# Performance work log

Measured on AMD Instinct MI355X. Metric: run time of the kernel, lower is better.

The kernel has to match this reference:

```python
import jax, jax.numpy as jnp
import numpy as np

SR = 48000
HARMONIC_NUM = 8          # -> 9 harmonics total
SINE_AMP = 0.1
NOISE_STD = 0.003
VOICED_THRESHOLD = 0.0
B, T, UPP = 8, 2000, 480
S = T * UPP


def setup_inputs() -> dict:
    key = jax.random.key(0)
    k_f0, k_mask, k_ri, k_noise = jax.random.split(key, 4)
    f0 = jax.random.uniform(k_f0, (B, 1, T), jnp.float32, 80.0, 500.0)
    voiced = (jax.random.uniform(k_mask, (B, 1, T)) > 0.2).astype(jnp.float32)
    f0 = f0 * voiced
    # random initial phases; harmonic 0 gets phase 0 (as in torch code)
    rand_ini = jax.random.uniform(k_ri, (B, HARMONIC_NUM + 1), jnp.float32)
    rand_ini = rand_ini.at[:, 0].set(0.0)
    noise_raw = jax.random.normal(k_noise, (B, S), jnp.float32)
    # linear mixing layer: weight = 1/(H+1), bias = 0 per nn.init in __init__
    w = jnp.full((HARMONIC_NUM + 1,), 1.0 / (HARMONIC_NUM + 1), jnp.float32)
    b = jnp.zeros((1,), jnp.float32)
    return {"f0": f0, "rand_ini": rand_ini, "noise_raw": noise_raw,
            "w": w, "b": b, "upp": UPP}


def reference(f0, rand_ini, noise_raw, w, b, upp):
    # f0: [B,1,T] Hz -> nearest-upsample to [B, S]
    f0u = jnp.repeat(f0[:, 0, :], upp, axis=1)              # [B, S]
    uv = (f0u > VOICED_THRESHOLD).astype(f0.dtype)          # [B, S]
    rad = f0u * (2.0 * np.pi / SR)
    # cumsum is linear: one cumsum, broadcast-multiply by harmonic index
    base_phase = jnp.cumsum(rad, axis=1)                    # [B, S]
    mult = jnp.arange(1, HARMONIC_NUM + 2, dtype=f0.dtype)  # [H+1]
    phase = base_phase[:, :, None] * mult + rand_ini[:, None, :] * (2.0 * np.pi)
    sines = jnp.sin(phase) * uv[:, :, None]                 # [B, S, H+1]
    har = jnp.tanh(sines @ w + b[0]) * SINE_AMP             # [B, S]
    noise = noise_raw * NOISE_STD                            # [B, S]
    return har[:, None, :], noise[:, None, :], uv[:, None, :]
```

## Files before the change

### kernel.cpp

```cpp
#include <hip/hip_runtime.h>
#include <hip/hip_bf16.h>
#include <math.h>

constexpr int   B_   = 8;
constexpr int   T_   = 2000;
constexpr int   UPP_ = 480;
constexpr int   S_   = T_ * UPP_;
constexpr int   NH   = 9;
constexpr int   SPT  = 8;
constexpr int   TPR  = S_ / SPT;
constexpr int   NT   = B_ * TPR;
constexpr float INV_SR = 1.0f / 48000.0f;

__global__ __launch_bounds__(256) void frame_scan_kernel(
    const float* __restrict__ f0,
    float2* __restrict__ ftab)
{
    __shared__ double wsum[4];
    const int b    = blockIdx.x;
    const int j    = threadIdx.x;
    const int lane = j & 63;
    const int wid  = j >> 6;
    constexpr int CH = 8;
    const int t0 = j * CH;

    float fc[CH];
    double local = 0.0;
    #pragma unroll
    for (int k = 0; k < CH; ++k) {
        int t = t0 + k;
        float v = (t < T_) ? f0[b * T_ + t] : 0.0f;
        fc[k] = v * INV_SR;
        local += (double)fc[k] * (double)UPP_;
    }

    double x = local;
    #pragma unroll
    for (int off = 1; off < 64; off <<= 1) {
        double y = __shfl_up(x, off, 64);
        if (lane >= off) x += y;
    }
    if (lane == 63) wsum[wid] = x;
    __syncthreads();

    double woff = 0.0;
    #pragma unroll
    for (int w = 0; w < 3; ++w)
        if (w < wid) woff += wsum[w];

    double excl = (x + woff) - local;

    #pragma unroll
    for (int k = 0; k < CH; ++k) {
        int t = t0 + k;
        if (t < T_) {
            double ph = excl - floor(excl);
            ftab[b * T_ + t] = make_float2((float)ph, fc[k]);
            excl += (double)fc[k] * (double)UPP_;
        }
    }
}

__global__ __launch_bounds__(256) void synth_kernel(
    const float* __restrict__ rand_ini,
    const float* __restrict__ noise_raw,
    const float* __restrict__ w,
    const float* __restrict__ bb,
    const float2* __restrict__ ftab,
    float* __restrict__ out)
{
    int g = blockIdx.x * blockDim.x + threadIdx.x;
    if (g >= NT) return;

    int b  = g / TPR;
    int r  = g - b * TPR;
    int s0 = r * SPT;
    int t  = s0 / UPP_;
    int i0 = s0 - t * UPP_;

    float2 pf   = ftab[b * T_ + t];
    float  Pred = pf.x;
    float  fcyc = pf.y;
    float  uvf  = (fcyc > 0.0f) ? 1.0f : 0.0f;
    float  bias = bb[0];

    const size_t row = (size_t)b * S_ + s0;
    const float4 nz0 = *(const float4*)(noise_raw + row);
    const float4 nz1 = *(const float4*)(noise_raw + row + 4);

    float har[SPT];

    if (uvf > 0.0f) {
        float wr[NH], ri[NH];
        #pragma unroll
        for (int h = 0; h < NH; ++h) {
            wr[h] = w[h];
            ri[h] = rand_ini[b * NH + h];
        }
        #pragma unroll
        for (int k = 0; k < SPT; ++k) {
            float base = Pred + fcyc * (float)(i0 + 1 + k);
            float acc = 0.0f;
            #pragma unroll
            for (int h = 0; h < NH; ++h) {
                float ph = base * (float)(h + 1) + ri[h];
                float fr = ph - floorf(ph);
#if __has_builtin(__builtin_amdgcn_sinf)
                float sv = __builtin_amdgcn_sinf(fr);
#else
                float sv = __sinf(fr * 6.2831853071795864769f);
#endif
                acc = fmaf(sv, wr[h], acc);
            }
            float xx = acc + bias;
            float e  = __expf(2.0f * xx);
            har[k]   = (e - 1.0f) / (e + 1.0f) * 0.1f;
        }
    } else {
        float e  = __expf(2.0f * bias);
        float hv = (e - 1.0f) / (e + 1.0f) * 0.1f;
        #pragma unroll
        for (int k = 0; k < SPT; ++k) har[k] = hv;
    }

    float* harp = out;
    float* nzp  = out + (size_t)B_ * S_;
    float* uvp  = out + (size_t)2 * B_ * S_;

    *(float4*)(harp + row)     = make_float4(har[0], har[1], har[2], har[3]);
    *(float4*)(harp + row + 4) = make_float4(har[4], har[5], har[6], har[7]);
    *(float4*)(nzp + row)      = make_float4(nz0.x * 0.003f, nz0.y * 0.003f,
                                             nz0.z * 0.003f, nz0.w * 0.003f);
    *(float4*)(nzp + row + 4)  = make_float4(nz1.x * 0.003f, nz1.y * 0.003f,
                                             nz1.z * 0.003f, nz1.w * 0.003f);
    *(float4*)(uvp + row)      = make_float4(uvf, uvf, uvf, uvf);
    *(float4*)(uvp + row + 4)  = make_float4(uvf, uvf, uvf, uvf);
}

extern "C" void kernel_launch(void* const* d_in, const int* in_sizes, int n_in,
                              void* d_out, int out_size, void* d_ws, size_t ws_size,
                              hipStream_t stream) {
    const float* f0        = (const float*)d_in[0];
    const float* rand_ini  = (const float*)d_in[1];
    const float* noise_raw = (const float*)d_in[2];
    const float* w         = (const float*)d_in[3];
    const float* bb        = (const float*)d_in[4];

    float2* ftab = (float2*)d_ws;

    frame_scan_kernel<<<B_, 256, 0, stream>>>(f0, ftab);
    synth_kernel<<<(NT + 255) / 256, 256, 0, stream>>>(
        rand_ini, noise_raw, w, bb, ftab, (float*)d_out);
}
```

Measured before the change: 34.45 us.

## Replace per-harmonic sines with Chebyshev recurrence and precomputed phase coefficients

Expands sin(h*theta + phi) as sin(h*theta)cos(phi) + cos(h*theta)sin(phi), so the mixing weights and random phases fold into A/B coefficient tables built once in the scan kernel. The harmonics come from a Chebyshev recurrence seeded by one sin/cos pair per sample, replacing nine transcendental calls and fracts. The change also raises samples per thread to 12 with 320-thread blocks aligned to rows, removes the voiced branch by masking the accumulator with uvf, and uses nontemporal loads and stores. The recurrence can accumulate float error at higher harmonics, and it drops the early skip of work for unvoiced frames.

```diff
diff --git a/kernel.cpp b/kernel.cpp
--- a/kernel.cpp
+++ b/kernel.cpp
@@ -7,14 +7,39 @@
 constexpr int   UPP_ = 480;
 constexpr int   S_   = T_ * UPP_;
 constexpr int   NH   = 9;
-constexpr int   SPT  = 8;
+constexpr int   SPT  = 12;
+constexpr int   BLK  = 320;
 constexpr int   TPR  = S_ / SPT;
-constexpr int   NT   = B_ * TPR;
+constexpr int   BPR  = TPR / BLK;
 constexpr float INV_SR = 1.0f / 48000.0f;
+
+typedef float fx4 __attribute__((ext_vector_type(4)));
+
+#if __has_builtin(__builtin_amdgcn_sinf)
+__device__ __forceinline__ float sinrev(float x) { return __builtin_amdgcn_sinf(x); }
+#else
+__device__ __forceinline__ float sinrev(float x) { return __sinf(x * 6.2831853071795864769f); }
+#endif
+#if __has_builtin(__builtin_amdgcn_cosf)
+__device__ __forceinline__ float cosrev(float x) { return __builtin_amdgcn_cosf(x); }
+#else
+__device__ __forceinline__ float cosrev(float x) { return __cosf(x * 6.2831853071795864769f); }
+#endif
+
+__device__ __forceinline__ void nt_store4(float* p, float a, float b, float c, float d) {
+    fx4 v = {a, b, c, d};
+    __builtin_nontemporal_store(v, (fx4*)p);
+}
+__device__ __forceinline__ fx4 nt_load4(const float* p) {
+    return __builtin_nontemporal_load((const fx4*)p);
+}
 
 __global__ __launch_bounds__(256) void frame_scan_kernel(
     const float* __restrict__ f0,
-    float2* __restrict__ ftab)
+    const float* __restrict__ rand_ini,
+    const float* __restrict__ w,
+    float2* __restrict__ ftab,
+    float2* __restrict__ abtab)
 {
     __shared__ double wsum[4];
     const int b    = blockIdx.x;
@@ -23,6 +48,12 @@
     const int wid  = j >> 6;
     constexpr int CH = 8;
     const int t0 = j * CH;
+
+    if (j < NH) {
+        float ri = rand_ini[b * NH + j];
+        float wv = w[j];
+        abtab[b * NH + j] = make_float2(wv * cosrev(ri), wv * sinrev(ri));
+    }
 
     float fc[CH];
     double local = 0.0;
@@ -45,8 +76,8 @@
 
     double woff = 0.0;
     #pragma unroll
-    for (int w = 0; w < 3; ++w)
-        if (w < wid) woff += wsum[w];
+    for (int ww = 0; ww < 3; ++ww)
+        if (ww < wid) woff += wsum[ww];
 
     double excl = (x + woff) - local;
 
@@ -61,80 +92,76 @@
     }
 }
 
-__global__ __launch_bounds__(256) void synth_kernel(
-    const float* __restrict__ rand_ini,
+__global__ __launch_bounds__(BLK) void synth_kernel(
     const float* __restrict__ noise_raw,
-    const float* __restrict__ w,
     const float* __restrict__ bb,
     const float2* __restrict__ ftab,
+    const float2* __restrict__ abtab,
     float* __restrict__ out)
 {
-    int g = blockIdx.x * blockDim.x + threadIdx.x;
-    if (g >= NT) return;
+    const int bblk = blockIdx.x / BPR;
+    const int rblk = blockIdx.x - bblk * BPR;
+    const int r    = rblk * BLK + threadIdx.x;
+    const int s0   = r * SPT;
+    const int t    = s0 / UPP_;
+    const int i0   = s0 - t * UPP_;
 
-    int b  = g / TPR;
-    int r  = g - b * TPR;
-    int s0 = r * SPT;
-    int t  = s0 / UPP_;
-    int i0 = s0 - t * UPP_;
+    float A[NH], Bc[NH];
+    #pragma unroll
+    for (int h = 0; h < NH; ++h) {
+        float2 ab = abtab[bblk * NH + h];
+        A[h]  = ab.x;
+        Bc[h] = ab.y;
+    }
+    const float bias = bb[0];
 
-    float2 pf   = ftab[b * T_ + t];
-    float  Pred = pf.x;
-    float  fcyc = pf.y;
-    float  uvf  = (fcyc > 0.0f) ? 1.0f : 0.0f;
-    float  bias = bb[0];
+    const float2 pf   = ftab[bblk * T_ + t];
+    const float  Pred = pf.x;
+    const float  fcyc = pf.y;
+    const float  uvf  = (fcyc > 0.0f) ? 1.0f : 0.0f;
 
-    const size_t row = (size_t)b * S_ + s0;
-    const float4 nz0 = *(const float4*)(noise_raw + row);
-    const float4 nz1 = *(const float4*)(noise_raw + row + 4);
+    const size_t row = (size_t)bblk * S_ + s0;
+    const fx4 nz0 = nt_load4(noise_raw + row);
+    const fx4 nz1 = nt_load4(noise_raw + row + 4);
+    const fx4 nz2 = nt_load4(noise_raw + row + 8);
 
     float har[SPT];
-
-    if (uvf > 0.0f) {
-        float wr[NH], ri[NH];
+    #pragma unroll
+    for (int k = 0; k < SPT; ++k) {
+        float base = Pred + fcyc * (float)(i0 + 1 + k);
+        float f    = base - floorf(base);
+        float s1   = sinrev(f);
+        float c1   = cosrev(f);
+        float tc   = c1 + c1;
+        float sm1 = 0.0f, cm1 = 1.0f;
+        float sm  = s1,   cm  = c1;
+        float acc = 0.0f;
         #pragma unroll
         for (int h = 0; h < NH; ++h) {
-            wr[h] = w[h];
-            ri[h] = rand_ini[b * NH + h];
+            acc = fmaf(sm, A[h], acc);
+            acc = fmaf(cm, Bc[h], acc);
+            float sn = fmaf(tc, sm, -sm1);
+            float cn = fmaf(tc, cm, -cm1);
+            sm1 = sm; cm1 = cm; sm = sn; cm = cn;
         }
-        #pragma unroll
-        for (int k = 0; k < SPT; ++k) {
-            float base = Pred + fcyc * (float)(i0 + 1 + k);
-            float acc = 0.0f;
-            #pragma unroll
-            for (int h = 0; h < NH; ++h) {
-                float ph = base * (float)(h + 1) + ri[h];
-                float fr = ph - floorf(ph);
-#if __has_builtin(__builtin_amdgcn_sinf)
-                float sv = __builtin_amdgcn_sinf(fr);
-#else
-                float sv = __sinf(fr * 6.2831853071795864769f);
-#endif
-                acc = fmaf(sv, wr[h], acc);
-            }
-            float xx = acc + bias;
-            float e  = __expf(2.0f * xx);
-            har[k]   = (e - 1.0f) / (e + 1.0f) * 0.1f;
-        }
-    } else {
-        float e  = __expf(2.0f * bias);
-        float hv = (e - 1.0f) / (e + 1.0f) * 0.1f;
-        #pragma unroll
-        for (int k = 0; k < SPT; ++k) har[k] = hv;
+        float xx = fmaf(acc, uvf, bias);
+        float e  = __expf(2.0f * xx);
+        har[k]   = (e - 1.0f) / (e + 1.0f) * 0.1f;
     }
 
     float* harp = out;
     float* nzp  = out + (size_t)B_ * S_;
     float* uvp  = out + (size_t)2 * B_ * S_;
 
-    *(float4*)(harp + row)     = make_float4(har[0], har[1], har[2], har[3]);
-    *(float4*)(harp + row + 4) = make_float4(har[4], har[5], har[6], har[7]);
-    *(float4*)(nzp + row)      = make_float4(nz0.x * 0.003f, nz0.y * 0.003f,
-                                             nz0.z * 0.003f, nz0.w * 0.003f);
-    *(float4*)(nzp + row + 4)  = make_float4(nz1.x * 0.003f, nz1.y * 0.003f,
-                                             nz1.z * 0.003f, nz1.w * 0.003f);
-    *(float4*)(uvp + row)      = make_float4(uvf, uvf, uvf, uvf);
-    *(float4*)(uvp + row + 4)  = make_float4(uvf, uvf, uvf, uvf);
+    nt_store4(harp + row,     har[0], har[1], har[2],  har[3]);
+    nt_store4(harp + row + 4, har[4], har[5], har[6],  har[7]);
+    nt_store4(harp + row + 8, har[8], har[9], har[10], har[11]);
+    nt_store4(nzp + row,     nz0.x * 0.003f, nz0.y * 0.003f, nz0.z * 0.003f, nz0.w * 0.003f);
+    nt_store4(nzp + row + 4, nz1.x * 0.003f, nz1.y * 0.003f, nz1.z * 0.003f, nz1.w * 0.003f);
+    nt_store4(nzp + row + 8, nz2.x * 0.003f, nz2.y * 0.003f, nz2.z * 0.003f, nz2.w * 0.003f);
+    nt_store4(uvp + row,     uvf, uvf, uvf, uvf);
+    nt_store4(uvp + row + 4, uvf, uvf, uvf, uvf);
+    nt_store4(uvp + row + 8, uvf, uvf, uvf, uvf);
 }
 
 extern "C" void kernel_launch(void* const* d_in, const int* in_sizes, int n_in,
@@ -146,9 +173,10 @@
     const float* w         = (const float*)d_in[3];
     const float* bb        = (const float*)d_in[4];
 
-    float2* ftab = (float2*)d_ws;
+    float2* ftab  = (float2*)d_ws;
+    float2* abtab = (float2*)((char*)d_ws + 128000);
 
-    frame_scan_kernel<<<B_, 256, 0, stream>>>(f0, ftab);
-    synth_kernel<<<(NT + 255) / 256, 256, 0, stream>>>(
-        rand_ini, noise_raw, w, bb, ftab, (float*)d_out);
+    frame_scan_kernel<<<B_, 256, 0, stream>>>(f0, rand_ini, w, ftab, abtab);
+    synth_kernel<<<B_ * BPR, BLK, 0, stream>>>(
+        noise_raw, bb, ftab, abtab, (float*)d_out);
 }
```

New measurement: 70.96 us. 106% more time.
